# Performance work log

Hardware: AMD Instinct MI355X
Metric: run time of the kernel (lower is better)

Reference implementation:

```python
import jax, jax.numpy as jnp
import numpy as np

B, S, F = 32, 8, 4
N0, N1, N2 = 2048, 4096, 2048
H, OUT = 1024, 256
IN = N0 + N1 + N2  # 8192
SC_LAYERS = 2


def setup_inputs() -> dict:
    key = jax.random.key(0)
    ks = jax.random.split(key, 16)
    rn = jax.random.normal
    inp = {
        'xs0': rn(ks[0], (B, S, N0), jnp.float32),
        'xs1': rn(ks[1], (B, S, N1), jnp.float32),
        'xs2': rn(ks[2], (B, S, N2), jnp.float32),
        # dense Laplacians, scaled so L@x keeps unit-ish variance
        'L0': rn(ks[3], (N0, N0), jnp.float32) / np.sqrt(N0).astype(np.float32),
        'L1': rn(ks[4], (N1, N1), jnp.float32) / np.sqrt(N1).astype(np.float32),
        'L2': rn(ks[5], (N2, N2), jnp.float32) / np.sqrt(N2).astype(np.float32),
        # per-layer, per-filter diagonal weights (std=0.01 as in torch init)
        'Wc0': 0.01 * rn(ks[6], (SC_LAYERS, F, N0), jnp.float32),
        'Wc1': 0.01 * rn(ks[7], (SC_LAYERS, F, N1), jnp.float32),
        'Wc2': 0.01 * rn(ks[8], (SC_LAYERS, F, N2), jnp.float32),
        # MLP params (xavier-ish)
        'W_in': rn(ks[9], (IN, H), jnp.float32) / np.sqrt(IN).astype(np.float32),
        'b_in': jnp.zeros((H,), jnp.float32),
        'W_h': rn(ks[10], (H, H), jnp.float32) / np.sqrt(H).astype(np.float32),
        'b_h': jnp.zeros((H,), jnp.float32),
        'W_out': rn(ks[11], (H, OUT), jnp.float32) / np.sqrt(H).astype(np.float32),
        'b_out': jnp.zeros((OUT,), jnp.float32),
    }
    return inp


def _conv_stack(x, L, Wc):
    # x: [B, S, n]; L: [n, n]; Wc: [layers, F, n]
    for l in range(Wc.shape[0]):
        # batched Laplacian matmul: (L @ x_bs) for every (b, s)
        Lx = jnp.einsum('bsn,mn->bsm', x, L)  # [B, S, n]
        # diagonal filter scaling + activation + sum over filters (fused)
        x = jax.nn.relu(Lx[:, :, None, :] * Wc[l][None, None, :, :]).sum(axis=2)
    return x


def reference(xs0, xs1, xs2, L0, L1, L2, Wc0, Wc1, Wc2,
              W_in, b_in, W_h, b_h, W_out, b_out):
    h = jnp.concatenate([
        _conv_stack(xs0, L0, Wc0),
        _conv_stack(xs1, L1, Wc1),
        _conv_stack(xs2, L2, Wc2),
    ], axis=-1)                      # [B, S, IN]
    h = h.sum(axis=1)                # sum over sequence -> [B, IN]
    h = jax.nn.relu(h @ W_in + b_in)
    h = jax.nn.relu(h @ W_h + b_h)   # single hidden layer (nn_layers=2)
    return h @ W_out + b_out         # [B, OUT]
```

## Files before the change

kernel.cpp:

```cpp
#include <hip/hip_runtime.h>
#include <hip/hip_bf16.h>


#define B_    32
#define S_    8
#define BS_   256
#define F_    4
#define IN_   8192
#define H_    1024
#define OUT_  256

#define L_TOT  25165824LL
#define LOFF1  4194304LL
#define LOFF2  20971520LL

typedef __attribute__((ext_vector_type(8)))  short bf16x8;
typedef __attribute__((ext_vector_type(4)))  short short4v;
typedef __attribute__((ext_vector_type(8)))  short short8v;
typedef __attribute__((ext_vector_type(16))) float f32x16;
typedef __attribute__((ext_vector_type(4)))  float f32x4;

typedef const __attribute__((address_space(1))) void* gas_ptr;
typedef __attribute__((address_space(3))) void* las_ptr;

__device__ __forceinline__ void gload16(const void* g, void* s) {
    __builtin_amdgcn_global_load_lds((gas_ptr)g, (las_ptr)s, 16, 0, 0);
}

__device__ __forceinline__ unsigned short rne_bf16(float f) {
    unsigned int u = __builtin_bit_cast(unsigned int, f);
    u += 0x7FFFu + ((u >> 16) & 1u);
    return (unsigned short)(u >> 16);
}

__global__ void k_pre(const float* __restrict__ L0, const float* __restrict__ L1,
                      const float* __restrict__ L2, unsigned short* __restrict__ Lb,
                      const float* __restrict__ x0, const float* __restrict__ x1,
                      const float* __restrict__ x2,
                      unsigned short* __restrict__ Xhi, unsigned short* __restrict__ Xlo,
                      const float* __restrict__ Wc0, const float* __restrict__ Wc1,
                      const float* __restrict__ Wc2, float* __restrict__ PM)
{
    const int bx = blockIdx.x, tid = threadIdx.x;
    if (bx < 3072) {
        const long long b0 = (long long)bx * 8192;
        const float* src; long long off;
        if (b0 < LOFF1)      { src = L0; off = 0; }
        else if (b0 < LOFF2) { src = L1; off = LOFF1; }
        else                 { src = L2; off = LOFF2; }
        const float* pb = src + (b0 - off) + tid * 8;
        #pragma unroll
        for (int u = 0; u < 4; ++u) {
            const float* p = pb + u * 2048;
            f32x4 a = __builtin_nontemporal_load((const f32x4*)p);
            f32x4 b = __builtin_nontemporal_load((const f32x4*)p + 1);
            short8v o;
            o[0] = (short)rne_bf16(a.x); o[1] = (short)rne_bf16(a.y);
            o[2] = (short)rne_bf16(a.z); o[3] = (short)rne_bf16(a.w);
            o[4] = (short)rne_bf16(b.x); o[5] = (short)rne_bf16(b.y);
            o[6] = (short)rne_bf16(b.z); o[7] = (short)rne_bf16(b.w);
            *(short8v*)(Lb + b0 + u * 2048 + tid * 8) = o;
        }
    } else if (bx < 3584) {
        const int base = (bx - 3072) * 4096 + tid * 8;
        #pragma unroll
        for (int u = 0; u < 2; ++u) {
            int e = base + u * 2048;
            int m = e >> 13, c = e & 8191;
            const float* src; int n, c0;
            if (c < 2048)      { src = x0; n = 2048; c0 = c; }
            else if (c < 6144) { src = x1; n = 4096; c0 = c - 2048; }
            else               { src = x2; n = 2048; c0 = c - 6144; }
            const float* p = src + (size_t)m * n + c0;
            f32x4 a = __builtin_nontemporal_load((const f32x4*)p);
            f32x4 b = __builtin_nontemporal_load((const f32x4*)p + 1);
            float v[8] = {a.x, a.y, a.z, a.w, b.x, b.y, b.z, b.w};
            short8v h, l;
            #pragma unroll
            for (int i = 0; i < 8; ++i) {
                unsigned short hb = rne_bf16(v[i]);
                float hf = __builtin_bit_cast(float, (unsigned int)hb << 16);
                h[i] = (short)hb;
                l[i] = (short)rne_bf16(v[i] - hf);
            }
            *(short8v*)(Xhi + (size_t)m * IN_ + c) = h;
            *(short8v*)(Xlo + (size_t)m * IN_ + c) = l;
        }
    } else {
        const int base = (bx - 3584) * 2048 + tid * 8;
        #pragma unroll
        for (int i = 0; i < 8; ++i) {
            int idx = base + i;
            int l = idx / IN_, n = idx % IN_;
            const float* Wc; int nb, j;
            if (n < 2048)      { Wc = Wc0; nb = 2048; j = n;        }
            else if (n < 6144) { Wc = Wc1; nb = 4096; j = n - 2048; }
            else               { Wc = Wc2; nb = 2048; j = n - 6144; }
            float p = 0.f, m = 0.f;
            #pragma unroll
            for (int f = 0; f < F_; ++f) {
                float w = Wc[(l * F_ + f) * nb + j];
                p += fmaxf(w, 0.f);
                m += fmaxf(-w, 0.f);
            }
            PM[(l * 2 + 0) * IN_ + n] = p;
            PM[(l * 2 + 1) * IN_ + n] = m;
        }
    }
}

__global__ __launch_bounds__(256, 2) void k_gemm(
    const unsigned short* __restrict__ Xhi, const unsigned short* __restrict__ Xlo,
    const unsigned short* __restrict__ Lb,
    float* __restrict__ pf)
{
    __shared__ __attribute__((aligned(16))) unsigned short Ah[3][128 * 32];
    __shared__ __attribute__((aligned(16))) unsigned short Al[3][128 * 32];
    __shared__ __attribute__((aligned(16))) unsigned short Bs[3][128 * 32];

    const int bx = blockIdx.x;
    const int idx = bx >> 1;
    int n_, noff, mt, nt, sk, k0, iters; long long loff;
    if ((bx & 1) == 0) {
        sk = idx & 3; int v = idx >> 2; mt = v & 1; nt = v >> 1;
        n_ = 4096; noff = 2048; loff = LOFF1; k0 = sk << 10; iters = 32;
    } else {
        if (idx < 128) { int u = idx;       sk = u & 3; int v = u >> 2; mt = v & 1; nt = v >> 1;
                         n_ = 2048; noff = 0; loff = 0; }
        else           { int u = idx - 128; sk = u & 3; int v = u >> 2; mt = v & 1; nt = v >> 1;
                         n_ = 2048; noff = 6144; loff = LOFF2; }
        k0 = sk << 9; iters = 16;
    }

    const int tid = threadIdx.x;

    const int sg = ((tid & 3) ^ ((tid >> 3) & 3)) << 3;
    const unsigned short* gAh = Xhi + (size_t)(mt * 128 + (tid >> 2)) * IN_ + noff + k0 + sg;
    const unsigned short* gAl = Xlo + (size_t)(mt * 128 + (tid >> 2)) * IN_ + noff + k0 + sg;
    const unsigned short* gB  = Lb + loff + (size_t)(nt * 128 + (tid >> 2)) * n_ + k0 + sg;
    const size_t a64 = (size_t)64 * IN_, b64 = (size_t)64 * n_;
    const int tb = tid * 16;

    char *aC = (char*)&Ah[0][0], *aN = (char*)&Ah[1][0], *aS = (char*)&Ah[2][0];
    char *lC = (char*)&Al[0][0], *lN = (char*)&Al[1][0], *lS = (char*)&Al[2][0];
    char *bC = (char*)&Bs[0][0], *bN = (char*)&Bs[1][0], *bS = (char*)&Bs[2][0];

    #define STAGE(pA, pL, pB, ko)                                  \
        do {                                                       \
            gload16(gAh + (ko),       (pA) + tb);                  \
            gload16(gAh + (ko) + a64, (pA) + 4096 + tb);           \
            gload16(gAl + (ko),       (pL) + tb);                  \
            gload16(gAl + (ko) + a64, (pL) + 4096 + tb);           \
            gload16(gB + (ko),        (pB) + tb);                  \
            gload16(gB + (ko) + b64,  (pB) + 4096 + tb);           \
        } while (0)

    const int l = tid & 63, w = tid >> 6;
    const int l31 = l & 31, lh = l >> 5;
    const int wm = w >> 1, wn = w & 1;
    const int swz = (l31 >> 1) & 3;
    const int ar0 = (wm * 64 + l31) * 32, ar1 = ar0 + 1024;
    const int br0 = (wn * 64 + l31) * 32, br1 = br0 + 1024;

    f32x16 a00, a01, a10, a11;
    #pragma unroll
    for (int r = 0; r < 16; ++r) { a00[r] = 0.f; a01[r] = 0.f; a10[r] = 0.f; a11[r] = 0.f; }

    STAGE(aC, lC, bC, 0);
    STAGE(aN, lN, bN, 32);

    for (int it = 0; it < iters; ++it) {
        if (it < iters - 1) asm volatile("s_waitcnt vmcnt(6)" ::: "memory");
        else                asm volatile("s_waitcnt vmcnt(0)" ::: "memory");
        __builtin_amdgcn_s_barrier();
        asm volatile("" ::: "memory");

        if (it + 2 < iters) STAGE(aS, lS, bS, (it + 2) * 32);
        __builtin_amdgcn_sched_barrier(0);

        const unsigned short* cA = (const unsigned short*)aC;
        const unsigned short* cL = (const unsigned short*)lC;
        const unsigned short* cB = (const unsigned short*)bC;
        __builtin_amdgcn_s_setprio(1);
        #pragma unroll
        for (int t = 0; t < 2; ++t) {
            const int sidx = (((t << 1) + lh) ^ swz) << 3;
            bf16x8 fah0 = *(const bf16x8*)&cA[ar0 + sidx];
            bf16x8 fah1 = *(const bf16x8*)&cA[ar1 + sidx];
            bf16x8 fal0 = *(const bf16x8*)&cL[ar0 + sidx];
            bf16x8 fal1 = *(const bf16x8*)&cL[ar1 + sidx];
            bf16x8 fb0  = *(const bf16x8*)&cB[br0 + sidx];
            bf16x8 fb1  = *(const bf16x8*)&cB[br1 + sidx];
            a00 = __builtin_amdgcn_mfma_f32_32x32x16_bf16(fal0, fb0, a00, 0, 0, 0);
            a00 = __builtin_amdgcn_mfma_f32_32x32x16_bf16(fah0, fb0, a00, 0, 0, 0);
            a01 = __builtin_amdgcn_mfma_f32_32x32x16_bf16(fal0, fb1, a01, 0, 0, 0);
            a01 = __builtin_amdgcn_mfma_f32_32x32x16_bf16(fah0, fb1, a01, 0, 0, 0);
            a10 = __builtin_amdgcn_mfma_f32_32x32x16_bf16(fal1, fb0, a10, 0, 0, 0);
            a10 = __builtin_amdgcn_mfma_f32_32x32x16_bf16(fah1, fb0, a10, 0, 0, 0);
            a11 = __builtin_amdgcn_mfma_f32_32x32x16_bf16(fal1, fb1, a11, 0, 0, 0);
            a11 = __builtin_amdgcn_mfma_f32_32x32x16_bf16(fah1, fb1, a11, 0, 0, 0);
        }
        __builtin_amdgcn_s_setprio(0);
        asm volatile("" ::: "memory");

        char* t1 = aC; aC = aN; aN = aS; aS = t1;
        char* t2 = lC; lC = lN; lN = lS; lS = t2;
        char* t3 = bC; bC = bN; bN = bS; bS = t3;
    }
    #undef STAGE

    const int colg = noff + nt * 128 + wn * 64 + l31;
    #pragma unroll
    for (int rb = 0; rb < 2; ++rb) {
        float* po = pf + ((size_t)sk * 256 + mt * 128 + wm * 64 + rb * 32 + 4 * lh) * IN_;
        const f32x16& c0 = rb ? a10 : a00;
        const f32x16& c1 = rb ? a11 : a01;
        #pragma unroll
        for (int e = 0; e < 16; ++e) {
            const int row = (e & 3) + 8 * (e >> 2);
            po[(size_t)row * IN_ + colg]      = c0[e];
            po[(size_t)row * IN_ + colg + 32] = c1[e];
        }
    }
}

__global__ void k_epi0(const float* __restrict__ pf,
                       const float* __restrict__ Pv, const float* __restrict__ Mv,
                       unsigned short* __restrict__ Yhi, unsigned short* __restrict__ Ylo) {
    int e = (blockIdx.x * 256 + threadIdx.x) * 4;
    int m = e >> 13, c = e & 8191;
    const float* p0 = pf + (size_t)m * IN_ + c;
    float vs[4] = {0.f, 0.f, 0.f, 0.f};
    #pragma unroll
    for (int s = 0; s < 4; ++s) {
        float4 v = *(const float4*)(p0 + (size_t)s * 256 * IN_);
        vs[0] += v.x; vs[1] += v.y; vs[2] += v.z; vs[3] += v.w;
    }
    float4 pv = *(const float4*)(Pv + c);
    float4 mv = *(const float4*)(Mv + c);
    float pa[4] = {pv.x, pv.y, pv.z, pv.w};
    float ma[4] = {mv.x, mv.y, mv.z, mv.w};
    short hv[4], lv[4];
    #pragma unroll
    for (int j = 0; j < 4; ++j) {
        float y = fmaxf(vs[j], 0.f) * pa[j] + fmaxf(-vs[j], 0.f) * ma[j];
        unsigned short hb = rne_bf16(y);
        float hf = __builtin_bit_cast(float, (unsigned int)hb << 16);
        hv[j] = (short)hb;
        lv[j] = (short)rne_bf16(y - hf);
    }
    short4v h = {hv[0], hv[1], hv[2], hv[3]};
    short4v lo = {lv[0], lv[1], lv[2], lv[3]};
    *(short4v*)(Yhi + (size_t)m * IN_ + c) = h;
    *(short4v*)(Ylo + (size_t)m * IN_ + c) = lo;
}

__global__ void k_epi1s(const float* __restrict__ pf,
                        const float* __restrict__ Pv, const float* __restrict__ Mv,
                        float* __restrict__ hsum) {
    int e = (blockIdx.x * 256 + threadIdx.x) * 4;
    int b = e >> 13, c = e & 8191;
    float4 pv = *(const float4*)(Pv + c);
    float4 mv = *(const float4*)(Mv + c);
    float pa[4] = {pv.x, pv.y, pv.z, pv.w};
    float ma[4] = {mv.x, mv.y, mv.z, mv.w};
    float hs[4] = {0.f, 0.f, 0.f, 0.f};
    for (int q = 0; q < 8; ++q) {
        const int m = b * 8 + q;
        const float* p0 = pf + (size_t)m * IN_ + c;
        float vs[4] = {0.f, 0.f, 0.f, 0.f};
        #pragma unroll
        for (int s = 0; s < 4; ++s) {
            float4 v = *(const float4*)(p0 + (size_t)s * 256 * IN_);
            vs[0] += v.x; vs[1] += v.y; vs[2] += v.z; vs[3] += v.w;
        }
        #pragma unroll
        for (int j = 0; j < 4; ++j)
            hs[j] += fmaxf(vs[j], 0.f) * pa[j] + fmaxf(-vs[j], 0.f) * ma[j];
    }
    *(float4*)(hsum + (size_t)b * IN_ + c) = *(float4*)hs;
}

template<int KC>
__global__ __launch_bounds__(256) void k_mlp3(
    const float* __restrict__ X, const float* __restrict__ W,
    float* __restrict__ P, int K, int H)
{
    __shared__ float Xs[32][KC];
    const int tid = threadIdx.x;
    const int lane = tid & 63;
    const int mg = tid >> 6;
    const int h = (blockIdx.x * 64 + lane) * 4;
    const int c = blockIdx.y, k0 = c * KC;

    for (int i = tid * 4; i < 32 * KC; i += 1024) {
        int m = i / KC, kk = i % KC;
        *(float4*)&Xs[m][kk] = *(const float4*)(X + (size_t)m * K + k0 + kk);
    }
    __syncthreads();

    float4 acc[8];
    #pragma unroll
    for (int m = 0; m < 8; ++m) acc[m] = {0.f, 0.f, 0.f, 0.f};

    const float* wp = W + (size_t)k0 * H + h;
    for (int kk = 0; kk < KC; kk += 4) {
        float4 w4[4];
        #pragma unroll
        for (int u = 0; u < 4; ++u)
            w4[u] = *(const float4*)(wp + (size_t)(kk + u) * H);
        #pragma unroll
        for (int m = 0; m < 8; ++m) {
            float4 xv = *(const float4*)&Xs[mg * 8 + m][kk];
            acc[m].x = fmaf(xv.x, w4[0].x, acc[m].x);
            acc[m].y = fmaf(xv.x, w4[0].y, acc[m].y);
            acc[m].z = fmaf(xv.x, w4[0].z, acc[m].z);
            acc[m].w = fmaf(xv.x, w4[0].w, acc[m].w);
            acc[m].x = fmaf(xv.y, w4[1].x, acc[m].x);
            acc[m].y = fmaf(xv.y, w4[1].y, acc[m].y);
            acc[m].z = fmaf(xv.y, w4[1].z, acc[m].z);
            acc[m].w = fmaf(xv.y, w4[1].w, acc[m].w);
            acc[m].x = fmaf(xv.z, w4[2].x, acc[m].x);
            acc[m].y = fmaf(xv.z, w4[2].y, acc[m].y);
            acc[m].z = fmaf(xv.z, w4[2].z, acc[m].z);
            acc[m].w = fmaf(xv.z, w4[2].w, acc[m].w);
            acc[m].x = fmaf(xv.w, w4[3].x, acc[m].x);
            acc[m].y = fmaf(xv.w, w4[3].y, acc[m].y);
            acc[m].z = fmaf(xv.w, w4[3].z, acc[m].z);
            acc[m].w = fmaf(xv.w, w4[3].w, acc[m].w);
        }
    }
    #pragma unroll
    for (int m = 0; m < 8; ++m)
        *(float4*)(P + ((size_t)c * 32 + mg * 8 + m) * H + h) = acc[m];
}

__global__ void k_reduce4(const float* __restrict__ P, const float* __restrict__ bias,
                          float* __restrict__ Y, int NC, int MH4, int H, int do_relu) {
    int idx = blockIdx.x * 256 + threadIdx.x;
    if (idx >= MH4) return;
    int h0 = (idx * 4) % H;
    float4 s = *(const float4*)(bias + h0);
    for (int c = 0; c < NC; ++c) {
        float4 v = *(const float4*)(P + (size_t)c * MH4 * 4 + (size_t)idx * 4);
        s.x += v.x; s.y += v.y; s.z += v.z; s.w += v.w;
    }
    if (do_relu) {
        s.x = fmaxf(s.x, 0.f); s.y = fmaxf(s.y, 0.f);
        s.z = fmaxf(s.z, 0.f); s.w = fmaxf(s.w, 0.f);
    }
    *(float4*)(Y + (size_t)idx * 4) = s;
}

extern "C" void kernel_launch(void* const* d_in, const int* in_sizes, int n_in,
                              void* d_out, int out_size, void* d_ws, size_t ws_size,
                              hipStream_t stream) {
    const float* xs0  = (const float*)d_in[0];
    const float* xs1  = (const float*)d_in[1];
    const float* xs2  = (const float*)d_in[2];
    const float* L0   = (const float*)d_in[3];
    const float* L1   = (const float*)d_in[4];
    const float* L2   = (const float*)d_in[5];
    const float* Wc0  = (const float*)d_in[6];
    const float* Wc1  = (const float*)d_in[7];
    const float* Wc2  = (const float*)d_in[8];
    const float* W_in = (const float*)d_in[9];
    const float* b_in = (const float*)d_in[10];
    const float* W_h  = (const float*)d_in[11];
    const float* b_h  = (const float*)d_in[12];
    const float* W_out= (const float*)d_in[13];
    const float* b_out= (const float*)d_in[14];

    char* w = (char*)d_ws;
    float*          PM  = (float*)w;          w += (size_t)4 * IN_ * 4;
    unsigned short* Lb  = (unsigned short*)w; w += (size_t)L_TOT * 2;
    unsigned short* Xhi = (unsigned short*)w; w += (size_t)BS_ * IN_ * 2;
    unsigned short* Xlo = (unsigned short*)w; w += (size_t)BS_ * IN_ * 2;
    unsigned short* Yhi = (unsigned short*)w; w += (size_t)BS_ * IN_ * 2;
    unsigned short* Ylo = (unsigned short*)w; w += (size_t)BS_ * IN_ * 2;
    float*          pf  = (float*)w;          w += (size_t)4 * BS_ * IN_ * 4;
    float*          hsum= (float*)w;          w += (size_t)32 * IN_ * 4;
    float*          p1  = pf;
    float*          h1  = (float*)w;          w += (size_t)32 * H_ * 4;
    float*          p2  = (float*)w;          w += (size_t)32 * 32 * H_ * 4;
    float*          h2  = (float*)w;          w += (size_t)32 * H_ * 4;
    float*          p3  = (float*)w;          w += (size_t)32 * 32 * OUT_ * 4;

    k_pre<<<3592, 256, 0, stream>>>(L0, L1, L2, Lb, xs0, xs1, xs2, Xhi, Xlo,
                                    Wc0, Wc1, Wc2, PM);

    k_gemm<<<512, 256, 0, stream>>>(Xhi, Xlo, Lb, pf);
    k_epi0<<<2048, 256, 0, stream>>>(pf, PM + 0 * IN_, PM + 1 * IN_, Yhi, Ylo);
    k_gemm<<<512, 256, 0, stream>>>(Yhi, Ylo, Lb, pf);
    k_epi1s<<<256, 256, 0, stream>>>(pf, PM + 2 * IN_, PM + 3 * IN_, hsum);

    {
        dim3 g(4, 128);
        k_mlp3<64><<<g, 256, 0, stream>>>(hsum, W_in, p1, IN_, H_);
        k_reduce4<<<32, 256, 0, stream>>>(p1, b_in, h1, 128, 8192, H_, 1);
    }
    {
        dim3 g(4, 32);
        k_mlp3<32><<<g, 256, 0, stream>>>(h1, W_h, p2, H_, H_);
        k_reduce4<<<32, 256, 0, stream>>>(p2, b_h, h2, 32, 8192, H_, 1);
    }
    {
        dim3 g(1, 32);
        k_mlp3<32><<<g, 256, 0, stream>>>(h2, W_out, p3, H_, OUT_);
        k_reduce4<<<8, 256, 0, stream>>>(p3, b_out, (float*)d_out, 32, 2048, OUT_, 0);
    }
}
```

Measured before the change: 207.9 us.

## Widen GEMM tile to 128x256, double-buffer, rebalance split-K with per-stack partial layout

Each GEMM block now covers 256 Laplacian rows instead of 128, with double rather than triple LDS buffering. Every block runs 16 k-iterations: the big N1 stack uses split-K 8 and the small stacks split-K 4, giving 384 blocks instead of 512. This doubles reuse of the hi/lo activation tiles. Partial sums move to a packed per-stack layout that the epilogues decode, and the second-layer inputs reuse the X buffers. The costs are more accumulator registers, an extra barrier per iteration, and a different occupancy and wave balance.

```diff
diff --git a/kernel.cpp b/kernel.cpp
--- a/kernel.cpp
+++ b/kernel.cpp
@@ -13,6 +13,10 @@
 #define L_TOT  25165824LL
 #define LOFF1  4194304LL
 #define LOFF2  20971520LL
+
+#define PF_B1  2097152LL
+#define PF_B2  10485760LL
+#define PF_TOT 12582912LL
 
 typedef __attribute__((ext_vector_type(8)))  short bf16x8;
 typedef __attribute__((ext_vector_type(4)))  short short4v;
@@ -114,114 +118,129 @@
     const unsigned short* __restrict__ Lb,
     float* __restrict__ pf)
 {
-    __shared__ __attribute__((aligned(16))) unsigned short Ah[3][128 * 32];
-    __shared__ __attribute__((aligned(16))) unsigned short Al[3][128 * 32];
-    __shared__ __attribute__((aligned(16))) unsigned short Bs[3][128 * 32];
+    __shared__ __attribute__((aligned(16))) unsigned short Ah[2][128 * 32];
+    __shared__ __attribute__((aligned(16))) unsigned short Al[2][128 * 32];
+    __shared__ __attribute__((aligned(16))) unsigned short Bs[2][256 * 32];
 
     const int bx = blockIdx.x;
-    const int idx = bx >> 1;
-    int n_, noff, mt, nt, sk, k0, iters; long long loff;
-    if ((bx & 1) == 0) {
-        sk = idx & 3; int v = idx >> 2; mt = v & 1; nt = v >> 1;
-        n_ = 4096; noff = 2048; loff = LOFF1; k0 = sk << 10; iters = 32;
+    int n_, noff, mt, nt, sk, ld; long long loff; size_t pbase;
+    if (bx < 256) {
+        int u = bx;
+        int j = (u & 7) | ((u >> 4) << 3);
+        nt = j >> 3; sk = j & 7; mt = (u >> 3) & 1;
+        n_ = 4096; noff = 2048; loff = LOFF1; pbase = PF_B1; ld = 4096;
+    } else if (bx < 320) {
+        int u = bx - 256;
+        int j = (u & 7) | ((u >> 4) << 3);
+        nt = j >> 2; sk = j & 3; mt = (u >> 3) & 1;
+        n_ = 2048; noff = 0; loff = 0; pbase = 0; ld = 2048;
     } else {
-        if (idx < 128) { int u = idx;       sk = u & 3; int v = u >> 2; mt = v & 1; nt = v >> 1;
-                         n_ = 2048; noff = 0; loff = 0; }
-        else           { int u = idx - 128; sk = u & 3; int v = u >> 2; mt = v & 1; nt = v >> 1;
-                         n_ = 2048; noff = 6144; loff = LOFF2; }
-        k0 = sk << 9; iters = 16;
-    }
+        int u = bx - 320;
+        int j = (u & 7) | ((u >> 4) << 3);
+        nt = j >> 2; sk = j & 3; mt = (u >> 3) & 1;
+        n_ = 2048; noff = 6144; loff = LOFF2; pbase = PF_B2; ld = 2048;
+    }
+    const int k0 = sk * 512;
 
     const int tid = threadIdx.x;
 
     const int sg = ((tid & 3) ^ ((tid >> 3) & 3)) << 3;
     const unsigned short* gAh = Xhi + (size_t)(mt * 128 + (tid >> 2)) * IN_ + noff + k0 + sg;
     const unsigned short* gAl = Xlo + (size_t)(mt * 128 + (tid >> 2)) * IN_ + noff + k0 + sg;
-    const unsigned short* gB  = Lb + loff + (size_t)(nt * 128 + (tid >> 2)) * n_ + k0 + sg;
+    const unsigned short* gB  = Lb + loff + (size_t)(nt * 256 + (tid >> 2)) * n_ + k0 + sg;
     const size_t a64 = (size_t)64 * IN_, b64 = (size_t)64 * n_;
     const int tb = tid * 16;
 
-    char *aC = (char*)&Ah[0][0], *aN = (char*)&Ah[1][0], *aS = (char*)&Ah[2][0];
-    char *lC = (char*)&Al[0][0], *lN = (char*)&Al[1][0], *lS = (char*)&Al[2][0];
-    char *bC = (char*)&Bs[0][0], *bN = (char*)&Bs[1][0], *bS = (char*)&Bs[2][0];
-
-    #define STAGE(pA, pL, pB, ko)                                  \
-        do {                                                       \
-            gload16(gAh + (ko),       (pA) + tb);                  \
-            gload16(gAh + (ko) + a64, (pA) + 4096 + tb);           \
-            gload16(gAl + (ko),       (pL) + tb);                  \
-            gload16(gAl + (ko) + a64, (pL) + 4096 + tb);           \
-            gload16(gB + (ko),        (pB) + tb);                  \
-            gload16(gB + (ko) + b64,  (pB) + 4096 + tb);           \
+    #define STAGE(buf, ko)                                                      \
+        do {                                                                    \
+            char* pa = (char*)&Ah[buf][0];                                      \
+            char* pl = (char*)&Al[buf][0];                                      \
+            char* pb = (char*)&Bs[buf][0];                                      \
+            gload16(gAh + (ko),       pa + tb);                                 \
+            gload16(gAh + (ko) + a64, pa + 4096 + tb);                          \
+            gload16(gAl + (ko),       pl + tb);                                 \
+            gload16(gAl + (ko) + a64, pl + 4096 + tb);                          \
+            gload16(gB + (ko),           pb + tb);                              \
+            gload16(gB + (ko) + b64,     pb + 4096 + tb);                       \
+            gload16(gB + (ko) + 2 * b64, pb + 8192 + tb);                       \
+            gload16(gB + (ko) + 3 * b64, pb + 12288 + tb);                      \
         } while (0)
 
     const int l = tid & 63, w = tid >> 6;
     const int l31 = l & 31, lh = l >> 5;
     const int wm = w >> 1, wn = w & 1;
     const int swz = (l31 >> 1) & 3;
-    const int ar0 = (wm * 64 + l31) * 32, ar1 = ar0 + 1024;
-    const int br0 = (wn * 64 + l31) * 32, br1 = br0 + 1024;
-
-    f32x16 a00, a01, a10, a11;
+
+    f32x16 acc[2][4];
     #pragma unroll
-    for (int r = 0; r < 16; ++r) { a00[r] = 0.f; a01[r] = 0.f; a10[r] = 0.f; a11[r] = 0.f; }
-
-    STAGE(aC, lC, bC, 0);
-    STAGE(aN, lN, bN, 32);
-
-    for (int it = 0; it < iters; ++it) {
-        if (it < iters - 1) asm volatile("s_waitcnt vmcnt(6)" ::: "memory");
-        else                asm volatile("s_waitcnt vmcnt(0)" ::: "memory");
+    for (int r = 0; r < 2; ++r)
+        #pragma unroll
+        for (int c = 0; c < 4; ++c)
+            #pragma unroll
+            for (int e = 0; e < 16; ++e) acc[r][c][e] = 0.f;
+
+    STAGE(0, 0);
+    STAGE(1, 32);
+
+    for (int it = 0; it < 16; ++it) {
+        if (it < 15) asm volatile("s_waitcnt vmcnt(8)" ::: "memory");
+        else         asm volatile("s_waitcnt vmcnt(0)" ::: "memory");
         __builtin_amdgcn_s_barrier();
         asm volatile("" ::: "memory");
 
-        if (it + 2 < iters) STAGE(aS, lS, bS, (it + 2) * 32);
-        __builtin_amdgcn_sched_barrier(0);
-
-        const unsigned short* cA = (const unsigned short*)aC;
-        const unsigned short* cL = (const unsigned short*)lC;
-        const unsigned short* cB = (const unsigned short*)bC;
+        const int cur = it & 1;
+        const unsigned short* cA = &Ah[cur][0];
+        const unsigned short* cL = &Al[cur][0];
+        const unsigned short* cB = &Bs[cur][0];
         __builtin_amdgcn_s_setprio(1);
         #pragma unroll
         for (int t = 0; t < 2; ++t) {
             const int sidx = (((t << 1) + lh) ^ swz) << 3;
-            bf16x8 fah0 = *(const bf16x8*)&cA[ar0 + sidx];
-            bf16x8 fah1 = *(const bf16x8*)&cA[ar1 + sidx];
-            bf16x8 fal0 = *(const bf16x8*)&cL[ar0 + sidx];
-            bf16x8 fal1 = *(const bf16x8*)&cL[ar1 + sidx];
-            bf16x8 fb0  = *(const bf16x8*)&cB[br0 + sidx];
-            bf16x8 fb1  = *(const bf16x8*)&cB[br1 + sidx];
-            a00 = __builtin_amdgcn_mfma_f32_32x32x16_bf16(fal0, fb0, a00, 0, 0, 0);
-            a00 = __builtin_amdgcn_mfma_f32_32x32x16_bf16(fah0, fb0, a00, 0, 0, 0);
-            a01 = __builtin_amdgcn_mfma_f32_32x32x16_bf16(fal0, fb1, a01, 0, 0, 0);
-            a01 = __builtin_amdgcn_mfma_f32_32x32x16_bf16(fah0, fb1, a01, 0, 0, 0);
-            a10 = __builtin_amdgcn_mfma_f32_32x32x16_bf16(fal1, fb0, a10, 0, 0, 0);
-            a10 = __builtin_amdgcn_mfma_f32_32x32x16_bf16(fah1, fb0, a10, 0, 0, 0);
-            a11 = __builtin_amdgcn_mfma_f32_32x32x16_bf16(fal1, fb1, a11, 0, 0, 0);
-            a11 = __builtin_amdgcn_mfma_f32_32x32x16_bf16(fah1, fb1, a11, 0, 0, 0);
+            bf16x8 fah[2], fal[2], fb[4];
+            #pragma unroll
+            for (int r = 0; r < 2; ++r) {
+                fah[r] = *(const bf16x8*)&cA[(wm * 64 + r * 32 + l31) * 32 + sidx];
+                fal[r] = *(const bf16x8*)&cL[(wm * 64 + r * 32 + l31) * 32 + sidx];
+            }
+            #pragma unroll
+            for (int c = 0; c < 4; ++c)
+                fb[c] = *(const bf16x8*)&cB[(wn * 128 + c * 32 + l31) * 32 + sidx];
+            #pragma unroll
+            for (int r = 0; r < 2; ++r)
+                #pragma unroll
+                for (int c = 0; c < 4; ++c) {
+                    acc[r][c] = __builtin_amdgcn_mfma_f32_32x32x16_bf16(fal[r], fb[c], acc[r][c], 0, 0, 0);
+                    acc[r][c] = __builtin_amdgcn_mfma_f32_32x32x16_bf16(fah[r], fb[c], acc[r][c], 0, 0, 0);
+                }
         }
         __builtin_amdgcn_s_setprio(0);
         asm volatile("" ::: "memory");
-
-        char* t1 = aC; aC = aN; aN = aS; aS = t1;
-        char* t2 = lC; lC = lN; lN = lS; lS = t2;
-        char* t3 = bC; bC = bN; bN = bS; bS = t3;
+        __builtin_amdgcn_s_barrier();
+
+        if (it + 2 < 16) STAGE(cur, (it + 2) * 32);
+        asm volatile("" ::: "memory");
     }
     #undef STAGE
 
-    const int colg = noff + nt * 128 + wn * 64 + l31;
+    const int colL = nt * 256 + wn * 128 + l31;
+    float* pw = pf + pbase + (size_t)sk * 256 * ld;
     #pragma unroll
-    for (int rb = 0; rb < 2; ++rb) {
-        float* po = pf + ((size_t)sk * 256 + mt * 128 + wm * 64 + rb * 32 + 4 * lh) * IN_;
-        const f32x16& c0 = rb ? a10 : a00;
-        const f32x16& c1 = rb ? a11 : a01;
+    for (int r = 0; r < 2; ++r) {
+        const int rowb = mt * 128 + wm * 64 + r * 32 + 4 * lh;
         #pragma unroll
         for (int e = 0; e < 16; ++e) {
-            const int row = (e & 3) + 8 * (e >> 2);
-            po[(size_t)row * IN_ + colg]      = c0[e];
-            po[(size_t)row * IN_ + colg + 32] = c1[e];
-        }
-    }
+            const int row = rowb + (e & 3) + 8 * (e >> 2);
+            #pragma unroll
+            for (int c = 0; c < 4; ++c)
+                pw[(size_t)row * ld + colL + c * 32] = acc[r][c][e];
+        }
+    }
+}
+
+__device__ __forceinline__ void pf_decode(int c, size_t& base, int& nsl, int& ld, int& cl) {
+    if (c < 2048)      { base = 0;      nsl = 4; ld = 2048; cl = c; }
+    else if (c < 6144) { base = PF_B1;  nsl = 8; ld = 4096; cl = c - 2048; }
+    else               { base = PF_B2;  nsl = 4; ld = 2048; cl = c - 6144; }
 }
 
 __global__ void k_epi0(const float* __restrict__ pf,
@@ -229,11 +248,13 @@
                        unsigned short* __restrict__ Yhi, unsigned short* __restrict__ Ylo) {
     int e = (blockIdx.x * 256 + threadIdx.x) * 4;
     int m = e >> 13, c = e & 8191;
-    const float* p0 = pf + (size_t)m * IN_ + c;
+    size_t base; int nsl, ld, cl;
+    pf_decode(c, base, nsl, ld, cl);
+    const float* p0 = pf + base + (size_t)m * ld + cl;
+    const size_t sstr = (size_t)256 * ld;
     float vs[4] = {0.f, 0.f, 0.f, 0.f};
-    #pragma unroll
-    for (int s = 0; s < 4; ++s) {
-        float4 v = *(const float4*)(p0 + (size_t)s * 256 * IN_);
+    for (int s = 0; s < nsl; ++s) {
+        float4 v = *(const float4*)(p0 + (size_t)s * sstr);
         vs[0] += v.x; vs[1] += v.y; vs[2] += v.z; vs[3] += v.w;
     }
     float4 pv = *(const float4*)(Pv + c);
@@ -260,6 +281,9 @@
                         float* __restrict__ hsum) {
     int e = (blockIdx.x * 256 + threadIdx.x) * 4;
     int b = e >> 13, c = e & 8191;
+    size_t base; int nsl, ld, cl;
+    pf_decode(c, base, nsl, ld, cl);
+    const size_t sstr = (size_t)256 * ld;
     float4 pv = *(const float4*)(Pv + c);
     float4 mv = *(const float4*)(Mv + c);
     float pa[4] = {pv.x, pv.y, pv.z, pv.w};
@@ -267,11 +291,10 @@
     float hs[4] = {0.f, 0.f, 0.f, 0.f};
     for (int q = 0; q < 8; ++q) {
         const int m = b * 8 + q;
-        const float* p0 = pf + (size_t)m * IN_ + c;
+        const float* p0 = pf + base + (size_t)m * ld + cl;
         float vs[4] = {0.f, 0.f, 0.f, 0.f};
-        #pragma unroll
-        for (int s = 0; s < 4; ++s) {
-            float4 v = *(const float4*)(p0 + (size_t)s * 256 * IN_);
+        for (int s = 0; s < nsl; ++s) {
+            float4 v = *(const float4*)(p0 + (size_t)s * sstr);
             vs[0] += v.x; vs[1] += v.y; vs[2] += v.z; vs[3] += v.w;
         }
         #pragma unroll
@@ -376,22 +399,22 @@
     unsigned short* Lb  = (unsigned short*)w; w += (size_t)L_TOT * 2;
     unsigned short* Xhi = (unsigned short*)w; w += (size_t)BS_ * IN_ * 2;
     unsigned short* Xlo = (unsigned short*)w; w += (size_t)BS_ * IN_ * 2;
-    unsigned short* Yhi = (unsigned short*)w; w += (size_t)BS_ * IN_ * 2;
-    unsigned short* Ylo = (unsigned short*)w; w += (size_t)BS_ * IN_ * 2;
-    float*          pf  = (float*)w;          w += (size_t)4 * BS_ * IN_ * 4;
+    float*          pf  = (float*)w;          w += (size_t)PF_TOT * 4;
     float*          hsum= (float*)w;          w += (size_t)32 * IN_ * 4;
     float*          p1  = pf;
     float*          h1  = (float*)w;          w += (size_t)32 * H_ * 4;
     float*          p2  = (float*)w;          w += (size_t)32 * 32 * H_ * 4;
     float*          h2  = (float*)w;          w += (size_t)32 * H_ * 4;
     float*          p3  = (float*)w;          w += (size_t)32 * 32 * OUT_ * 4;
+    unsigned short* Yhi = Xhi;
+    unsigned short* Ylo = Xlo;
 
     k_pre<<<3592, 256, 0, stream>>>(L0, L1, L2, Lb, xs0, xs1, xs2, Xhi, Xlo,
                                     Wc0, Wc1, Wc2, PM);
 
-    k_gemm<<<512, 256, 0, stream>>>(Xhi, Xlo, Lb, pf);
+    k_gemm<<<384, 256, 0, stream>>>(Xhi, Xlo, Lb, pf);
     k_epi0<<<2048, 256, 0, stream>>>(pf, PM + 0 * IN_, PM + 1 * IN_, Yhi, Ylo);
-    k_gemm<<<512, 256, 0, stream>>>(Yhi, Ylo, Lb, pf);
+    k_gemm<<<384, 256, 0, stream>>>(Yhi, Ylo, Lb, pf);
     k_epi1s<<<256, 256, 0, stream>>>(pf, PM + 2 * IN_, PM + 3 * IN_, hsum);
 
     {
```

Result: slower. 223.2 us (+7.4%).
